# Kernel optimization log

Hardware: AMD Instinct MI355X
Metric: run time of the kernel (lower is better)

## Reference

```python
import jax, jax.numpy as jnp
import numpy as np

HIDDEN = 512
N_DRUG = 2000
N_REACTION = 10000
N_EDGES = 400000


def setup_inputs() -> dict:
    key = jax.random.key(0)
    ks = jax.random.split(key, 6)
    z_drug = jax.random.normal(ks[0], (N_DRUG, HIDDEN), dtype=jnp.float32)
    z_reaction = jax.random.normal(ks[1], (N_REACTION, HIDDEN), dtype=jnp.float32)
    row = jax.random.randint(ks[2], (N_EDGES,), 0, N_DRUG, dtype=jnp.int64)
    col = jax.random.randint(ks[3], (N_EDGES,), 0, N_REACTION, dtype=jnp.int64)
    # Linear weights in torch layout: (out_features, in_features)
    W1 = jax.random.normal(ks[4], (HIDDEN, 2 * HIDDEN), dtype=jnp.float32) * (1.0 / np.sqrt(2 * HIDDEN))
    b1 = jnp.zeros((HIDDEN,), dtype=jnp.float32)
    W2 = jax.random.normal(ks[5], (1, HIDDEN), dtype=jnp.float32) * (1.0 / np.sqrt(HIDDEN))
    b2 = jnp.zeros((1,), dtype=jnp.float32)
    return {"z_drug": z_drug, "z_reaction": z_reaction, "row": row, "col": col,
            "W1": W1, "b1": b1, "W2": W2, "b2": b2}


def reference(z_drug, z_reaction, row, col, W1, b1, W2, b2):
    # gather + concat: [E, 2H]
    z = jnp.concatenate([z_drug[row], z_reaction[col]], axis=-1)
    h = jax.nn.relu(jnp.einsum('eh,oh->eo', z, W1) + b1)  # [E, H]
    out = jnp.einsum('eh,oh->eo', h, W2) + b2             # [E, 1]
    return out.reshape(-1)
```

## Files before the change

### kernel.cpp

```cpp
#include <hip/hip_runtime.h>
#include <stdint.h>

#define HIDDEN 512
#define NDRUG 2000
#define NREACT 10000
#define NEDGE 400000

#define NBKT 250
#define HRROWS 40
#define SLOT 2048
#define CSTRIDE 16
#define NSCAT 128
#define EPB ((NEDGE + NSCAT - 1) / NSCAT)

#define BPB2 2
#define EBLK (NBKT * BPB2)
#define MAXSL 1024
#define HRSTRIDE 520
#define ETHREADS 512

__device__ __forceinline__ int col2bkt(int c) { return (c * 6554) >> 18; }

typedef __attribute__((ext_vector_type(8))) _Float16 f16x8;
typedef __attribute__((ext_vector_type(2))) _Float16 f16x2;
typedef __attribute__((ext_vector_type(4))) float f32x4;
typedef __attribute__((ext_vector_type(8))) float f32x8;
typedef __attribute__((ext_vector_type(4))) float float4v;
typedef __attribute__((ext_vector_type(4))) _Float16 f16x4;

#if defined(__has_builtin)
#if __has_builtin(__builtin_amdgcn_fdot2)
#define HAVE_FDOT2 1
#endif
#endif

__global__ __launch_bounds__(256) void w1prep(const float* __restrict__ W1,
                                              _Float16* __restrict__ WL,
                                              _Float16* __restrict__ WR,
                                              int* __restrict__ cursor) {
  const int b = blockIdx.x;
  const int tid = threadIdx.x;
  if (b < 128) {
    const int nth = 128 * 256;
    const int NQ = HIDDEN * 2 * HIDDEN / 4;
    for (int i = b * 256 + tid; i < NQ; i += nth) {
      int e = i * 4;
      int o = e >> 10, j = e & 1023;
      float4v v = *reinterpret_cast<const float4v*>(W1 + e);
      f16x4 q; q[0]=(_Float16)v[0]; q[1]=(_Float16)v[1]; q[2]=(_Float16)v[2]; q[3]=(_Float16)v[3];
      if (j < HIDDEN) *reinterpret_cast<f16x4*>(WL + o * HIDDEN + j) = q;
      else            *reinterpret_cast<f16x4*>(WR + o * HIDDEN + (j - HIDDEN)) = q;
    }
  } else {
    int i = (b - 128) * 256 + tid;
    if (i < NBKT) cursor[i * CSTRIDE] = i * SLOT;
  }
}

#define BM 64
#define BN 128
#define BK 32
#define GEMMBLKS 756

__global__ __launch_bounds__(256) void gemm_scatter(
    const float* __restrict__ z_drug, const float* __restrict__ z_react,
    const _Float16* __restrict__ BL, const _Float16* __restrict__ BR,
    const float* __restrict__ bias,
    const int* __restrict__ row, const int* __restrict__ col,
    _Float16* __restrict__ Hd, _Float16* __restrict__ Hr,
    int* __restrict__ cursor, uint64_t* __restrict__ pk)
{
  __shared__ _Float16 As[BM * BK];
  __shared__ _Float16 Bs[BN * BK];
  __shared__ int lhist[256];
  __shared__ int lbase[256];

  const int bid = blockIdx.x;
  const int tid = threadIdx.x;

  if (bid >= GEMMBLKS) {
    const int sb = bid - GEMMBLKS;
    const int e0 = sb * EPB;
    const int e1 = (e0 + EPB < NEDGE) ? e0 + EPB : NEDGE;
    if (tid < 256) { lhist[tid] = 0; }
    __syncthreads();
    for (int e = e0 + tid; e < e1; e += 256)
      atomicAdd(&lhist[col2bkt(col[e])], 1);
    __syncthreads();
    if (tid < NBKT) {
      int cnt = lhist[tid];
      lbase[tid] = cnt ? atomicAdd(&cursor[tid * CSTRIDE], cnt) : 0;
      lhist[tid] = 0;
    }
    __syncthreads();
    for (int e = e0 + tid; e < e1; e += 256) {
      int c = col[e];
      int r = row[e];
      int bkt = col2bkt(c);
      int lo = atomicAdd(&lhist[bkt], 1);
      pk[lbase[bkt] + lo] = ((uint64_t)e << 25) | ((uint64_t)r << 14) | (uint64_t)c;
    }
    return;
  }

  const int z = (bid >= 128) ? 1 : 0;
  const int t = z ? bid - 128 : bid;
  const int mb = t >> 2;
  const int nb = t & 3;
  const int M = (z == 0) ? NDRUG : NREACT;
  const float* A = (z == 0) ? z_drug : z_react;
  const _Float16* B = (z == 0) ? BL : BR;
  _Float16* C = (z == 0) ? Hd : Hr;
  const bool has_bias = (z == 0);
  const int K = HIDDEN, N = HIDDEN;

  const int lane = tid & 63;
  const int wid = tid >> 6;
  const int wn = wid;

  f32x4 acc[4][2];
#pragma unroll
  for (int i = 0; i < 4; ++i)
#pragma unroll
    for (int j = 0; j < 2; ++j) acc[i][j] = (f32x4){0.f, 0.f, 0.f, 0.f};

  const int row0 = mb * BM;
  const int col0 = nb * BN;
  const int r0 = tid >> 2;
  const int q0 = tid & 3;
  const int srow = lane >> 2;
  const int scol = (lane & 3) * 8;

  for (int kt = 0; kt < K; kt += BK) {
    int rA = row0 + r0;
    rA = rA < M ? rA : M - 1;
    f32x8 va = *reinterpret_cast<const f32x8*>(A + (size_t)rA * K + kt + q0 * 8);
    f16x8 afh = __builtin_convertvector(va, f16x8);
    __syncthreads();
    *reinterpret_cast<f16x8*>(As + r0 * BK + q0 * 8) = afh;
#pragma unroll
    for (int i = 0; i < 2; ++i) {
      int rB = col0 + wid * 32 + i * 16 + srow;
      const _Float16* gB = B + (size_t)rB * K + kt + scol;
      _Float16* lB = Bs + (wid * 32 + i * 16) * BK;
      __builtin_amdgcn_global_load_lds(
          (const __attribute__((address_space(1))) void*)gB,
          (__attribute__((address_space(3))) void*)lB, 16, 0, 0);
    }
    __syncthreads();

    const int fr = lane & 15;
    const int kg = (lane >> 4) * 8;
    f16x8 af[4], bfr[2];
#pragma unroll
    for (int mi = 0; mi < 4; ++mi)
      af[mi] = *reinterpret_cast<const f16x8*>(As + (mi * 16 + fr) * BK + kg);
#pragma unroll
    for (int ni = 0; ni < 2; ++ni)
      bfr[ni] = *reinterpret_cast<const f16x8*>(Bs + (wn * 32 + ni * 16 + fr) * BK + kg);
#pragma unroll
    for (int mi = 0; mi < 4; ++mi)
#pragma unroll
      for (int ni = 0; ni < 2; ++ni)
        acc[mi][ni] = __builtin_amdgcn_mfma_f32_16x16x32_f16(af[mi], bfr[ni], acc[mi][ni], 0, 0, 0);
  }

  const int crow = (lane >> 4) * 4;
  const int ccol = lane & 15;
#pragma unroll
  for (int ni = 0; ni < 2; ++ni) {
    const int gc = col0 + wn * 32 + ni * 16 + ccol;
    const float bv = has_bias ? bias[gc] : 0.0f;
#pragma unroll
    for (int mi = 0; mi < 4; ++mi) {
#pragma unroll
      for (int j = 0; j < 4; ++j) {
        const int gr = row0 + mi * 16 + crow + j;
        if (gr < M) C[(size_t)gr * N + gc] = (_Float16)(acc[mi][ni][j] + bv);
      }
    }
  }
}

__global__ __launch_bounds__(ETHREADS) void edge_kernel(
    const _Float16* __restrict__ Hd, const _Float16* __restrict__ Hr,
    const uint64_t* __restrict__ pk, const int* __restrict__ cursor,
    const float* __restrict__ W2, const float* __restrict__ b2,
    float* __restrict__ out)
{
  __shared__ _Float16 hrs[HRROWS * HRSTRIDE];
  __shared__ uint64_t spk[MAXSL];
  __shared__ int qdesc[MAXSL / 4 + HRROWS];
  __shared__ int cnt[HRROWS], cb[HRROWS], cnt2[HRROWS], qoff[HRROWS];
  __shared__ int nqs;

  const int bid = blockIdx.x;
  const int porig = bid >> 1;
  const int slice = bid & 1;
  const int xcd = porig & 7;
  const int pidx = porig >> 3;
  const int bucket = (xcd < 2 ? xcd * 32 : 2 * 32 + (xcd - 2) * 31) + pidx;
  const int cbase = bucket * HRROWS;
  const int base = bucket * SLOT;
  const int count = cursor[bucket * CSTRIDE] - base;
  const int per = (count + BPB2 - 1) / BPB2;
  const int s = slice * per;
  const int e_end0 = (s + per < count) ? s + per : count;
  const int n = (e_end0 > s) ? e_end0 - s : 0;

  const int tid = threadIdx.x;
  const int lane = tid & 63;
  const int li = lane & 15;
  const int wv = tid >> 6;
  const int gid = wv * 4 + (lane >> 4);

#pragma unroll
  for (int rr2 = 0; rr2 < 5; ++rr2) {
    int rr = wv * 5 + rr2;
    int gr = cbase + rr;
    const _Float16* src = Hr + (size_t)gr * HIDDEN + lane * 8;
    _Float16* dst = hrs + rr * HRSTRIDE;
    __builtin_amdgcn_global_load_lds(
        (const __attribute__((address_space(1))) void*)src,
        (__attribute__((address_space(3))) void*)dst, 16, 0, 0);
  }

  f16x8 w2v[4];
#pragma unroll
  for (int k = 0; k < 4; ++k) {
    const float* p = W2 + li * 8 + k * 128;
    f16x8 q;
#pragma unroll
    for (int j = 0; j < 8; ++j) q[j] = (_Float16)p[j];
    w2v[k] = q;
  }
  const float bias2 = *b2;
  const f16x8 zero8 = (f16x8)(_Float16)0;

  if (tid < HRROWS) { cnt[tid] = 0; cnt2[tid] = 0; }
  __syncthreads();
  uint64_t p0 = 0, p1 = 0;
  int b0 = 0, b1 = 0;
  const int i0 = tid, i1 = tid + ETHREADS;
  if (i0 < n) {
    p0 = pk[base + s + i0];
    b0 = (int)(p0 & 0x3FFF) - cbase;
    atomicAdd(&cnt[b0], 1);
  }
  if (i1 < n) {
    p1 = pk[base + s + i1];
    b1 = (int)(p1 & 0x3FFF) - cbase;
    atomicAdd(&cnt[b1], 1);
  }
  __syncthreads();
  if (tid == 0) {
    int acc = 0, qa = 0;
    for (int j = 0; j < HRROWS; ++j) {
      cb[j] = acc; acc += cnt[j];
      qoff[j] = qa; qa += (cnt[j] + 3) >> 2;
    }
    nqs = qa;
  }
  __syncthreads();
  if (i0 < n) { int lo = atomicAdd(&cnt2[b0], 1); spk[cb[b0] + lo] = p0; }
  if (i1 < n) { int lo = atomicAdd(&cnt2[b1], 1); spk[cb[b1] + lo] = p1; }
  __syncthreads();
  if (tid < HRROWS) {
    int j = tid, st = cb[j], len = cnt[j], o = qoff[j];
    for (int q = 0; q < len; q += 4) {
      int cn = len - q; cn = (cn < 4) ? cn : 4;
      qdesc[o++] = j | ((st + q) << 6) | (cn << 17);
    }
  }
  __syncthreads();

  const int nq = nqs;
  for (int q = gid; q < nq; q += 32) {
    const int d = qdesc[q];
    const int lc = d & 63;
    const int st = (d >> 6) & 2047;
    const int cn = (d >> 17) & 7;

    const _Float16* hd[4];
    int si[4];
#pragma unroll
    for (int j = 0; j < 4; ++j) {
      int jj = (j < cn) ? j : cn - 1;
      uint64_t p = spk[st + jj];
      si[j] = (int)(p >> 25);
      hd[j] = Hd + (size_t)((p >> 14) & 0x7FF) * HIDDEN;
    }

    f16x8 vd[4][4];
#pragma unroll
    for (int j = 0; j < 4; ++j)
#pragma unroll
      for (int k = 0; k < 4; ++k)
        vd[j][k] = *reinterpret_cast<const f16x8*>(hd[j] + li * 8 + k * 128);

    f16x8 hv[4];
#pragma unroll
    for (int k = 0; k < 4; ++k)
      hv[k] = *reinterpret_cast<const f16x8*>(hrs + lc * HRSTRIDE + li * 8 + k * 128);

    float acc[4] = {0.f, 0.f, 0.f, 0.f};
#pragma unroll
    for (int j = 0; j < 4; ++j) {
#pragma unroll
      for (int k = 0; k < 4; ++k) {
        f16x8 t = __builtin_elementwise_max(vd[j][k] + hv[k], zero8);
#if defined(HAVE_FDOT2)
#pragma unroll
        for (int qq = 0; qq < 4; ++qq) {
          f16x2 wp = {w2v[k][2 * qq], w2v[k][2 * qq + 1]};
          f16x2 sp = {t[2 * qq], t[2 * qq + 1]};
          acc[j] = __builtin_amdgcn_fdot2(sp, wp, acc[j], false);
        }
#else
#pragma unroll
        for (int qq = 0; qq < 8; ++qq)
          acc[j] += (float)t[qq] * (float)w2v[k][qq];
#endif
      }
    }
#pragma unroll
    for (int off = 8; off >= 1; off >>= 1) {
#pragma unroll
      for (int j = 0; j < 4; ++j) acc[j] += __shfl_xor(acc[j], off);
    }
    if (li == 0) {
      for (int j = 0; j < cn; ++j) out[si[j]] = acc[j] + bias2;
    }
  }
}

extern "C" void kernel_launch(void* const* d_in, const int* in_sizes, int n_in,
                              void* d_out, int out_size, void* d_ws, size_t ws_size,
                              hipStream_t stream) {
  const float* z_drug  = (const float*)d_in[0];
  const float* z_react = (const float*)d_in[1];
  const int*   row     = (const int*)d_in[2];
  const int*   col     = (const int*)d_in[3];
  const float* W1      = (const float*)d_in[4];
  const float* b1      = (const float*)d_in[5];
  const float* W2      = (const float*)d_in[6];
  const float* b2      = (const float*)d_in[7];
  float* out = (float*)d_out;

  char* ws = (char*)d_ws;
  size_t off = 0;
  auto alloc = [&](size_t bytes) {
    void* p = ws + off;
    off += (bytes + 255) & ~(size_t)255;
    return p;
  };
  _Float16* wl_f = (_Float16*)alloc((size_t)HIDDEN * HIDDEN * 2);
  _Float16* wr_f = (_Float16*)alloc((size_t)HIDDEN * HIDDEN * 2);
  _Float16* Hd   = (_Float16*)alloc((size_t)NDRUG * HIDDEN * 2);
  _Float16* Hr   = (_Float16*)alloc((size_t)NREACT * HIDDEN * 2);
  int*      cursor = (int*)alloc((size_t)NBKT * CSTRIDE * 4);
  uint64_t* pk     = (uint64_t*)alloc((size_t)NBKT * SLOT * 8);

  w1prep<<<130, 256, 0, stream>>>(W1, wl_f, wr_f, cursor);
  gemm_scatter<<<GEMMBLKS + NSCAT, 256, 0, stream>>>(z_drug, z_react, wl_f, wr_f, b1,
                                                     row, col, Hd, Hr, cursor, pk);
  edge_kernel<<<EBLK, ETHREADS, 0, stream>>>(Hd, Hr, pk, cursor, W2, b2, out);
}
```

Measured before the change: 62.88 us.

## Double-buffer GEMM LDS tiles and parallelize bucket prefix scan

New measurement: 61.52 us (median of 2 runs). 2.2% less time.

```diff
diff --git a/kernel.cpp b/kernel.cpp
--- a/kernel.cpp
+++ b/kernel.cpp
@@ -61,6 +61,8 @@
 #define BN 128
 #define BK 32
 #define GEMMBLKS 756
+#define ABUF (BM * BK)
+#define BBUF (BN * BK)
 
 __global__ __launch_bounds__(256) void gemm_scatter(
     const float* __restrict__ z_drug, const float* __restrict__ z_react,
@@ -70,8 +72,8 @@
     _Float16* __restrict__ Hd, _Float16* __restrict__ Hr,
     int* __restrict__ cursor, uint64_t* __restrict__ pk)
 {
-  __shared__ _Float16 As[BM * BK];
-  __shared__ _Float16 Bs[BN * BK];
+  __shared__ _Float16 As[2 * ABUF];
+  __shared__ _Float16 Bs[2 * BBUF];
   __shared__ int lhist[256];
   __shared__ int lbase[256];
 
@@ -104,15 +106,16 @@
   }
 
   const int z = (bid >= 128) ? 1 : 0;
-  const int t = z ? bid - 128 : bid;
-  const int mb = t >> 2;
-  const int nb = t & 3;
+  const int t0 = z ? bid - 128 : bid;
+  const int mb = t0 >> 2;
+  const int nb = t0 & 3;
   const int M = (z == 0) ? NDRUG : NREACT;
   const float* A = (z == 0) ? z_drug : z_react;
   const _Float16* B = (z == 0) ? BL : BR;
   _Float16* C = (z == 0) ? Hd : Hr;
   const bool has_bias = (z == 0);
   const int K = HIDDEN, N = HIDDEN;
+  const int NT = K / BK;
 
   const int lane = tid & 63;
   const int wid = tid >> 6;
@@ -131,33 +134,54 @@
   const int srow = lane >> 2;
   const int scol = (lane & 3) * 8;
 
-  for (int kt = 0; kt < K; kt += BK) {
-    int rA = row0 + r0;
-    rA = rA < M ? rA : M - 1;
-    f32x8 va = *reinterpret_cast<const f32x8*>(A + (size_t)rA * K + kt + q0 * 8);
-    f16x8 afh = __builtin_convertvector(va, f16x8);
-    __syncthreads();
-    *reinterpret_cast<f16x8*>(As + r0 * BK + q0 * 8) = afh;
+  int rA = row0 + r0;
+  rA = rA < M ? rA : M - 1;
+  const float* Arow = A + (size_t)rA * K + q0 * 8;
+
+  {
+    f32x8 va0 = *reinterpret_cast<const f32x8*>(Arow + 0);
+    *reinterpret_cast<f16x8*>(As + r0 * BK + q0 * 8) = __builtin_convertvector(va0, f16x8);
 #pragma unroll
     for (int i = 0; i < 2; ++i) {
       int rB = col0 + wid * 32 + i * 16 + srow;
-      const _Float16* gB = B + (size_t)rB * K + kt + scol;
+      const _Float16* gB = B + (size_t)rB * K + 0 + scol;
       _Float16* lB = Bs + (wid * 32 + i * 16) * BK;
       __builtin_amdgcn_global_load_lds(
           (const __attribute__((address_space(1))) void*)gB,
           (__attribute__((address_space(3))) void*)lB, 16, 0, 0);
     }
+  }
+  f32x8 va_n = *reinterpret_cast<const f32x8*>(Arow + BK);
+
+  const int fr = lane & 15;
+  const int kg = (lane >> 4) * 8;
+
+  for (int t = 0; t < NT; ++t) {
+    const int cur = t & 1;
     __syncthreads();
-
-    const int fr = lane & 15;
-    const int kg = (lane >> 4) * 8;
+    if (t < NT - 1) {
+      const int ktn = (t + 1) * BK;
+#pragma unroll
+      for (int i = 0; i < 2; ++i) {
+        int rB = col0 + wid * 32 + i * 16 + srow;
+        const _Float16* gB = B + (size_t)rB * K + ktn + scol;
+        _Float16* lB = Bs + (cur ^ 1) * BBUF + (wid * 32 + i * 16) * BK;
+        __builtin_amdgcn_global_load_lds(
+            (const __attribute__((address_space(1))) void*)gB,
+            (__attribute__((address_space(3))) void*)lB, 16, 0, 0);
+      }
+      *reinterpret_cast<f16x8*>(As + (cur ^ 1) * ABUF + r0 * BK + q0 * 8) =
+          __builtin_convertvector(va_n, f16x8);
+      if (t < NT - 2)
+        va_n = *reinterpret_cast<const f32x8*>(Arow + (t + 2) * BK);
+    }
     f16x8 af[4], bfr[2];
 #pragma unroll
     for (int mi = 0; mi < 4; ++mi)
-      af[mi] = *reinterpret_cast<const f16x8*>(As + (mi * 16 + fr) * BK + kg);
+      af[mi] = *reinterpret_cast<const f16x8*>(As + cur * ABUF + (mi * 16 + fr) * BK + kg);
 #pragma unroll
     for (int ni = 0; ni < 2; ++ni)
-      bfr[ni] = *reinterpret_cast<const f16x8*>(Bs + (wn * 32 + ni * 16 + fr) * BK + kg);
+      bfr[ni] = *reinterpret_cast<const f16x8*>(Bs + cur * BBUF + (wn * 32 + ni * 16 + fr) * BK + kg);
 #pragma unroll
     for (int mi = 0; mi < 4; ++mi)
 #pragma unroll
@@ -253,13 +277,19 @@
     atomicAdd(&cnt[b1], 1);
   }
   __syncthreads();
-  if (tid == 0) {
-    int acc = 0, qa = 0;
-    for (int j = 0; j < HRROWS; ++j) {
-      cb[j] = acc; acc += cnt[j];
-      qoff[j] = qa; qa += (cnt[j] + 3) >> 2;
-    }
-    nqs = qa;
+  if (tid < 64) {
+    int j = tid;
+    int c = (j < HRROWS) ? cnt[j] : 0;
+    int qc = (c + 3) >> 2;
+    int ic = c, iq = qc;
+#pragma unroll
+    for (int off = 1; off < 64; off <<= 1) {
+      int u = __shfl_up(ic, off);
+      int v = __shfl_up(iq, off);
+      if (lane >= off) { ic += u; iq += v; }
+    }
+    if (j < HRROWS) { cb[j] = ic - c; qoff[j] = iq - qc; }
+    if (j == HRROWS - 1) nqs = iq;
   }
   __syncthreads();
   if (i0 < n) { int lo = atomicAdd(&cnt2[b0], 1); spk[cb[b0] + lo] = p0; }
@@ -275,8 +305,12 @@
   __syncthreads();
 
   const int nq = nqs;
-  for (int q = gid; q < nq; q += 32) {
-    const int d = qdesc[q];
+  int q = gid;
+  int d = (q < nq) ? qdesc[q] : 0;
+  while (q < nq) {
+    const int qn = q + 32;
+    const int dn = (qn < nq) ? qdesc[qn] : 0;
+
     const int lc = d & 63;
     const int st = (d >> 6) & 2047;
     const int cn = (d >> 17) & 7;
@@ -331,6 +365,7 @@
     if (li == 0) {
       for (int j = 0; j < cn; ++j) out[si[j]] = acc[j] + bias2;
     }
+    q = qn; d = dn;
   }
 }
 
```
